# Kernel tuning notes

Hardware: AMD Instinct MI355X
Metric: run time of the kernel (lower is better)

The kernel has to match this reference:

```python
import jax, jax.numpy as jnp
import numpy as np

B, W, C, C2, K_DIV = 4, 64, 256, 256, 8
DPROJ = C // K_DIV  # 32


def setup_inputs() -> dict:
    key = jax.random.key(0)
    k1, k2, k3, k4 = jax.random.split(key, 4)
    x = jax.random.normal(k1, (B, W, W, C), dtype=jnp.float32)
    input_h = jax.random.normal(k2, (B, W, W, C2), dtype=jnp.float32)
    f_w = jax.random.normal(k3, (1, 1, C2, DPROJ), dtype=jnp.float32) * 0.05
    g_w = jax.random.normal(k4, (1, 1, C, DPROJ), dtype=jnp.float32) * 0.05
    return {"x": x, "input_h": input_h, "f_w": f_w, "g_w": g_w}


def reference(x, input_h, f_w, g_w):
    b, w, _, c = x.shape
    c2 = input_h.shape[-1]
    # 1x1 convs == channel matmuls
    f = jnp.einsum('bhwc,cd->bhwd', input_h, f_w[0, 0])   # [B,W,W,Dp]
    g = jnp.einsum('bhwc,cd->bhwd', x, g_w[0, 0])          # [B,W,W,Dp]
    gf = g.reshape(b, w * w, -1)                            # [B,N,Dp]
    ff = f.reshape(b, w * w, -1)                            # [B,N,Dp]
    s = jnp.einsum('bnd,bmd->bnm', gf, ff)                  # unscaled QK^T
    beta = jax.nn.softmax(s, axis=-1)
    hf = input_h.reshape(b, w * w, c2)                      # [B,N,C2]
    o = jnp.einsum('bnm,bmc->bnc', beta, hf).reshape(b, w, w, c2)
    return jnp.concatenate([o, x], axis=-1)                 # [B,W,W,C2+C]
```

## Files before the change

### kernel.cpp

```cpp
#include <hip/hip_runtime.h>
#include <hip/hip_bf16.h>

#define NB   4
#define NROW 4096
#define CIN  256
#define OUTC 512
#define DP   32
#define LOG2E 1.4426950408889634f

typedef __bf16 bf16x8 __attribute__((ext_vector_type(8)));
typedef float  f32x4  __attribute__((ext_vector_type(4)));
typedef float  f32x16 __attribute__((ext_vector_type(16)));
typedef ushort ushort8 __attribute__((ext_vector_type(8)));

#define MFMA32(a, b, c) __builtin_amdgcn_mfma_f32_32x32x16_bf16((a), (b), (c), 0, 0, 0)

__device__ __forceinline__ ushort f2bf(float x) {
  union { float f; unsigned u; } v; v.f = x;
  unsigned r = v.u + 0x7fffu + ((v.u >> 16) & 1u);
  return (ushort)(r >> 16);
}

__device__ __forceinline__ uint pack2(float a, float b) {
  __hip_bfloat162 h = __float22bfloat162_rn(float2{a, b});
  uint u; __builtin_memcpy(&u, &h, 4);
  return u;
}

__device__ __forceinline__ bf16x8 mk8(uint a, uint b, uint c, uint d) {
  uint tmp[4] = {a, b, c, d};
  bf16x8 r; __builtin_memcpy(&r, tmp, 16);
  return r;
}

__device__ __forceinline__ float fexp2(float x) {
  return __builtin_amdgcn_exp2f(x);
}

__device__ __forceinline__ void gload_lds16(const void* g, void* l) {
  __builtin_amdgcn_global_load_lds(
      (const __attribute__((address_space(1))) unsigned int*)g,
      (__attribute__((address_space(3))) unsigned int*)l, 16, 0, 0);
}


__global__ __launch_bounds__(256) void proj_mfma(
    const float* __restrict__ x, const float* __restrict__ h,
    const float* __restrict__ fw, const float* __restrict__ gw,
    ushort* __restrict__ Qb, ushort* __restrict__ Kb, ushort* __restrict__ Vw,
    float* __restrict__ out) {
  __shared__ ushort Ab[64 * 256];
  __shared__ ushort Wt[32 * 256];
  const int t = threadIdx.x;
  const int which = blockIdx.y;
  const float* in   = which ? h : x;
  const float* wsrc = which ? fw : gw;
  ushort* dst = which ? Kb : Qb;
  const float qsc = which ? 1.f : LOG2E;
  const int row0 = blockIdx.x * 64;

  {
    const float4* inp = (const float4*)(in + (size_t)row0 * CIN);
#pragma unroll
    for (int i = 0; i < 16; ++i) {
      const int idx = i * 256 + t;
      const int r = idx >> 6;
      const int c = (idx & 63) * 4;
      const float4 v = inp[idx];
      if (!which)
        ((float4*)(out + (size_t)(row0 + r) * OUTC + 256))[idx & 63] = v;
      ushort tmp[4] = {f2bf(v.x), f2bf(v.y), f2bf(v.z), f2bf(v.w)};
      const int slot = (c >> 3) ^ (r & 7);
      *(uint2*)&Ab[r * 256 + (slot << 3) + (c & 7)] = *(const uint2*)tmp;
    }
  }
  {
    const int d = t & 31;
    const int k0 = (t >> 5) * 32;
#pragma unroll 8
    for (int j = 0; j < 32; ++j)
      Wt[d * 256 + k0 + j] = f2bf(wsrc[(size_t)(k0 + j) * DP + d]);
  }
  __syncthreads();

  const int w = t >> 6, l = t & 63, lo = l & 15, hi = l >> 4;
  f32x4 acc[2];
  acc[0] = (f32x4){0.f, 0.f, 0.f, 0.f};
  acc[1] = (f32x4){0.f, 0.f, 0.f, 0.f};
  const int R = w * 16 + lo;
#pragma unroll
  for (int kk = 0; kk < 8; ++kk) {
    const int slot = (kk * 4 + hi) ^ (R & 7);
    const bf16x8 a = *(const bf16x8*)&Ab[R * 256 + (slot << 3)];
#pragma unroll
    for (int nt = 0; nt < 2; ++nt) {
      const bf16x8 bfr = *(const bf16x8*)&Wt[(nt * 16 + lo) * 256 + kk * 32 + hi * 8];
      acc[nt] = __builtin_amdgcn_mfma_f32_16x16x32_bf16(a, bfr, acc[nt], 0, 0, 0);
    }
  }
#pragma unroll
  for (int nt = 0; nt < 2; ++nt)
#pragma unroll
    for (int r = 0; r < 4; ++r)
      dst[(size_t)(row0 + w * 16 + hi * 4 + r) * DP + nt * 16 + lo] =
          f2bf(acc[nt][r] * qsc);

  if (which) {
    const int b = row0 >> 12;
    const int tile = (row0 & 4095) >> 6;
    const int c = t;
    ushort* vdst = Vw + (size_t)(b * 64 + tile) * 16384;
#pragma unroll
    for (int kt = 0; kt < 4; ++kt)
#pragma unroll
      for (int s2 = 0; s2 < 2; ++s2) {
        const int kbase = 16 * kt + 8 * (s2 ^ (c & 1));
        ushort tmp[8];
#pragma unroll
        for (int j = 0; j < 8; ++j) {
          const int slot = (c >> 3) ^ j;
          tmp[j] = Ab[(kbase + j) * 256 + (slot << 3) + (c & 7)];
        }
        *(ushort8*)(vdst + kt * 4096 + c * 16 + s2 * 8) = *(const ushort8*)tmp;
      }
  }
}

__global__ __launch_bounds__(256, 2) void attn32f(
    const ushort* __restrict__ Qb, const ushort* __restrict__ Kb,
    const ushort* __restrict__ Vw, float* __restrict__ pml,
    ushort* __restrict__ pacc) {
  __shared__ ushort Vt[2][16384];

  const int t  = threadIdx.x;
  const int w  = t >> 6;
  const int l  = t & 63;
  const int qq = l & 31;
  const int h  = l >> 5;

  const int bid = blockIdx.x;
  const int s   = bid & 3;
  const int b   = (bid >> 2) & 3;
  const int q0  = (bid >> 4) * 128 + w * 32;
  const size_t rbase = (size_t)b * NROW;

  bf16x8 qf0 = *(const bf16x8*)(Qb + (rbase + q0 + qq) * DP + h * 8);
  bf16x8 qf1 = *(const bf16x8*)(Qb + (rbase + q0 + qq) * DP + 16 + h * 8);

  f32x16 acc[8];
#pragma unroll
  for (int i = 0; i < 8; ++i) acc[i] = (f32x16){};
  float lsum = 0.f;

  const int tI0 = s * 16;
  const int vlane = qq * 32 + ((h ^ (qq & 1)) << 4);

  const int ko00 = qq * DP + h * 8;
  const int ko01 = qq * DP + 16 + h * 8;
  const int ko10 = (32 + qq) * DP + h * 8;
  const int ko11 = (32 + qq) * DP + 16 + h * 8;
  const ushort* kfp  = Kb + (rbase + (size_t)(tI0 + 1) * 64) * DP;
  const ushort* vsrc = Vw + (size_t)(b * 64 + tI0 + 1) * 16384;

  {
    const ushort* src0 = Vw + (size_t)(b * 64 + tI0) * 16384;
#pragma unroll
    for (int i = 0; i < 8; ++i)
      gload_lds16(src0 + (w * 8 + i) * 512 + l * 8, &Vt[0][(w * 8 + i) * 512]);
  }
  bf16x8 kf00, kf01, kf10, kf11;
  {
    const ushort* k0 = Kb + (rbase + (size_t)tI0 * 64) * DP;
    kf00 = *(const bf16x8*)(k0 + ko00);
    kf01 = *(const bf16x8*)(k0 + ko01);
    kf10 = *(const bf16x8*)(k0 + ko10);
    kf11 = *(const bf16x8*)(k0 + ko11);
  }
  __syncthreads();
  int cur = 0;

  for (int tt = 0; tt < 16; ++tt) {
    if (tt < 15) {
      ushort* dstl = &Vt[cur ^ 1][0];
#pragma unroll
      for (int i = 0; i < 8; ++i)
        gload_lds16(vsrc + (w * 8 + i) * 512 + l * 8, dstl + (w * 8 + i) * 512);
    }

    f32x16 st0 = (f32x16){}, st1 = (f32x16){};
    st0 = MFMA32(kf00, qf0, st0);
    st0 = MFMA32(kf01, qf1, st0);
    st1 = MFMA32(kf10, qf0, st1);
    st1 = MFMA32(kf11, qf1, st1);

#pragma unroll
    for (int i = 0; i < 16; ++i) st0[i] = fexp2(st0[i]);
    float s0;
    {
      float sm[8];
#pragma unroll
      for (int i = 0; i < 8; ++i) sm[i] = st0[i] + st0[i + 8];
#pragma unroll
      for (int d = 4; d >= 1; d >>= 1)
#pragma unroll
        for (int i = 0; i < d; ++i) sm[i] += sm[i + d];
      s0 = sm[0];
    }
    bf16x8 pb0, pb1;
    {
      const uint a00 = pack2(st0[0],  st0[1]),  a01 = pack2(st0[2],  st0[3]);
      const uint a10 = pack2(st0[4],  st0[5]),  a11 = pack2(st0[6],  st0[7]);
      const uint a20 = pack2(st0[8],  st0[9]),  a21 = pack2(st0[10], st0[11]);
      const uint a30 = pack2(st0[12], st0[13]), a31 = pack2(st0[14], st0[15]);
      auto p0 = __builtin_amdgcn_permlane32_swap(a00, a10, false, false);
      auto p1 = __builtin_amdgcn_permlane32_swap(a01, a11, false, false);
      auto p2 = __builtin_amdgcn_permlane32_swap(a20, a30, false, false);
      auto p3 = __builtin_amdgcn_permlane32_swap(a21, a31, false, false);
      pb0 = mk8(p0[0], p1[0], p0[1], p1[1]);
      pb1 = mk8(p2[0], p3[0], p2[1], p3[1]);
    }

    const char* vb = (const char*)&Vt[cur][0] + vlane;
    __builtin_amdgcn_s_setprio(1);
#pragma unroll
    for (int ct = 0; ct < 8; ++ct) {
      const bf16x8 v0 = *(const bf16x8*)(vb + ct * 1024);
      const bf16x8 v1 = *(const bf16x8*)(vb + 8192 + ct * 1024);
      acc[ct] = MFMA32(v0, pb0, acc[ct]);
      st1[2 * ct] = fexp2(st1[2 * ct]);
      acc[ct] = MFMA32(v1, pb1, acc[ct]);
      st1[2 * ct + 1] = fexp2(st1[2 * ct + 1]);
    }
    bf16x8 pb2, pb3;
    {
      const uint b00 = pack2(st1[0],  st1[1]),  b01 = pack2(st1[2],  st1[3]);
      const uint b10 = pack2(st1[4],  st1[5]),  b11 = pack2(st1[6],  st1[7]);
      const uint b20 = pack2(st1[8],  st1[9]),  b21 = pack2(st1[10], st1[11]);
      const uint b30 = pack2(st1[12], st1[13]), b31 = pack2(st1[14], st1[15]);
      auto p4 = __builtin_amdgcn_permlane32_swap(b00, b10, false, false);
      auto p5 = __builtin_amdgcn_permlane32_swap(b01, b11, false, false);
      auto p6 = __builtin_amdgcn_permlane32_swap(b20, b30, false, false);
      auto p7 = __builtin_amdgcn_permlane32_swap(b21, b31, false, false);
      pb2 = mk8(p4[0], p5[0], p4[1], p5[1]);
      pb3 = mk8(p6[0], p7[0], p6[1], p7[1]);
    }

    float s1 = 0.f;
#pragma unroll
    for (int ct = 0; ct < 8; ++ct) {
      const bf16x8 v2 = *(const bf16x8*)(vb + 16384 + ct * 1024);
      const bf16x8 v3 = *(const bf16x8*)(vb + 24576 + ct * 1024);
      acc[ct] = MFMA32(v2, pb2, acc[ct]);
      if (ct == 0) kf00 = *(const bf16x8*)(kfp + ko00);
      if (ct == 1) kf01 = *(const bf16x8*)(kfp + ko01);
      if (ct == 2) kf10 = *(const bf16x8*)(kfp + ko10);
      if (ct == 3) kf11 = *(const bf16x8*)(kfp + ko11);
      acc[ct] = MFMA32(v3, pb3, acc[ct]);
      s1 += st1[2 * ct] + st1[2 * ct + 1];
    }
    __builtin_amdgcn_s_setprio(0);
    lsum += s0 + s1;

    __syncthreads();
    cur ^= 1;
    kfp += 64 * DP;
    vsrc += 16384;
  }

  lsum += __shfl_xor(lsum, 32, 64);
  const size_t prow = rbase + q0 + qq;
  if (h == 0) pml[prow * 4 + s] = lsum;
  ushort* pr = pacc + (prow * 4 + s) * 256;
#pragma unroll
  for (int ct = 0; ct < 8; ++ct)
#pragma unroll
    for (int j = 0; j < 4; ++j) {
      uint2 d;
      d.x = pack2(acc[ct][4 * j], acc[ct][4 * j + 1]);
      d.y = pack2(acc[ct][4 * j + 2], acc[ct][4 * j + 3]);
      *(uint2*)&pr[ct * 32 + j * 8 + h * 4] = d;
    }
}

__global__ __launch_bounds__(256) void reduce_o(
    const float* __restrict__ pml, const ushort* __restrict__ pacc,
    float* __restrict__ out) {
  const int t = threadIdx.x;
  const int row = blockIdx.x * 8 + (t >> 5);
  const int c0 = (t & 31) * 8;

  const float L = pml[row * 4] + pml[row * 4 + 1] + pml[row * 4 + 2] + pml[row * 4 + 3];
  float o[8] = {0.f, 0.f, 0.f, 0.f, 0.f, 0.f, 0.f, 0.f};
#pragma unroll
  for (int s = 0; s < 4; ++s) {
    const bf16x8 a = *(const bf16x8*)(pacc + ((size_t)row * 4 + s) * 256 + c0);
#pragma unroll
    for (int i = 0; i < 8; ++i) o[i] += (float)a[i];
  }
  const float inv = 1.f / L;
  float4 o0 = {o[0] * inv, o[1] * inv, o[2] * inv, o[3] * inv};
  float4 o1 = {o[4] * inv, o[5] * inv, o[6] * inv, o[7] * inv};
  float4* op = (float4*)(out + (size_t)row * OUTC + c0);
  op[0] = o0; op[1] = o1;
}

__global__ __launch_bounds__(256) void proj_fb(
    const float* __restrict__ x, const float* __restrict__ h,
    const float* __restrict__ fw, const float* __restrict__ gw,
    float* __restrict__ out) {
  __shared__ float wl[8192];
  __shared__ float rows[8][260];
  const int t = threadIdx.x;
  const int which = blockIdx.y;
  const float* in = which ? h : x;
  const float* w  = which ? fw : gw;
  for (int i = t; i < 8192; i += 256) wl[i] = w[i];
  const int row0 = blockIdx.x * 32;
  const int d = t & 31, rl = t >> 5;
  for (int rp = 0; rp < 4; ++rp) {
    __syncthreads();
    for (int i = t; i < 2048; i += 256)
      rows[i >> 8][i & 255] = in[(long)(row0 + rp * 8 + (i >> 8)) * CIN + (i & 255)];
    __syncthreads();
    float a = 0.f;
#pragma unroll 8
    for (int c = 0; c < 256; ++c) a = fmaf(rows[rl][c], wl[c * 32 + d], a);
    const long row = row0 + rp * 8 + rl;
    ((ushort*)(out + row * OUTC + 256))[which * 32 + d] = f2bf(a);
  }
}

__global__ __launch_bounds__(256) void attn_fb(
    const float* __restrict__ h, float* __restrict__ out) {
  __shared__ alignas(16) ushort Vt[256][72];
  __shared__ alignas(16) ushort Pl[4][16][72];
  const int t = threadIdx.x;
  const int w = t >> 6, l = t & 63, lo = l & 15, hi = l >> 4;
  const int bid = blockIdx.x;
  const int b = (bid >> 1) & 3;
  const int qb = ((bid >> 3) << 1) | (bid & 1);
  const int q0 = qb * 64;
  const long rowbase = (long)b * NROW;
  const ushort* gslot = (const ushort*)(out + (rowbase + q0 + w * 16 + lo) * OUTC + 256);
  const bf16x8 qf = *(const bf16x8*)(gslot + hi * 8);
  f32x4 acc[16];
#pragma unroll
  for (int i = 0; i < 16; ++i) acc[i] = (f32x4){0.f, 0.f, 0.f, 0.f};
  float mrow[4] = {-1e30f, -1e30f, -1e30f, -1e30f};
  float lsum[4] = {0.f, 0.f, 0.f, 0.f};
  for (int k0 = 0; k0 < NROW; k0 += 64) {
    bf16x8 kf[4];
#pragma unroll
    for (int kt = 0; kt < 4; ++kt) {
      const ushort* fslot =
          (const ushort*)(out + (rowbase + k0 + kt * 16 + lo) * OUTC + 256) + 32;
      kf[kt] = *(const bf16x8*)(fslot + hi * 8);
    }
    __syncthreads();
    {
      const float* hp = h + (rowbase + k0) * CIN + t;
#pragma unroll
      for (int g8 = 0; g8 < 8; ++g8) {
        ushort tmp[8];
#pragma unroll
        for (int i = 0; i < 8; ++i) tmp[i] = f2bf(hp[(g8 * 8 + i) * CIN]);
        *(bf16x8*)&Vt[t][g8 * 8] = *(const bf16x8*)tmp;
      }
    }
    __syncthreads();
    f32x4 sv[4];
#pragma unroll
    for (int kt = 0; kt < 4; ++kt)
      sv[kt] = __builtin_amdgcn_mfma_f32_16x16x32_bf16(
          qf, kf[kt], (f32x4){0.f, 0.f, 0.f, 0.f}, 0, 0, 0);
    float alpha[4];
    bool upd = false;
#pragma unroll
    for (int r = 0; r < 4; ++r) {
      float m4 = fmaxf(fmaxf(sv[0][r], sv[1][r]), fmaxf(sv[2][r], sv[3][r]));
#pragma unroll
      for (int off = 1; off < 16; off <<= 1) m4 = fmaxf(m4, __shfl_xor(m4, off, 64));
      const float mn = fmaxf(mrow[r], m4);
      alpha[r] = __expf(mrow[r] - mn);
      upd |= (mn > mrow[r]);
      mrow[r] = mn;
    }
    if (__any(upd)) {
#pragma unroll
      for (int ct = 0; ct < 16; ++ct)
#pragma unroll
        for (int r = 0; r < 4; ++r) acc[ct][r] *= alpha[r];
#pragma unroll
      for (int r = 0; r < 4; ++r) lsum[r] *= alpha[r];
    }
#pragma unroll
    for (int r = 0; r < 4; ++r) {
      float ps = 0.f;
#pragma unroll
      for (int kt = 0; kt < 4; ++kt) {
        const float p = __expf(sv[kt][r] - mrow[r]);
        sv[kt][r] = p;
        ps += p;
      }
#pragma unroll
      for (int off = 1; off < 16; off <<= 1) ps += __shfl_xor(ps, off, 64);
      lsum[r] += ps;
    }
#pragma unroll
    for (int kt = 0; kt < 4; ++kt)
#pragma unroll
      for (int r = 0; r < 4; ++r)
        Pl[w][hi * 4 + r][kt * 16 + lo] = f2bf(sv[kt][r]);
    asm volatile("s_waitcnt lgkmcnt(0)" ::: "memory");
    const bf16x8 pa0 = *(const bf16x8*)&Pl[w][lo][hi * 8];
    const bf16x8 pa1 = *(const bf16x8*)&Pl[w][lo][32 + hi * 8];
#pragma unroll
    for (int ct = 0; ct < 16; ++ct) {
      const bf16x8 v0 = *(const bf16x8*)&Vt[ct * 16 + lo][hi * 8];
      const bf16x8 v1 = *(const bf16x8*)&Vt[ct * 16 + lo][32 + hi * 8];
      acc[ct] = __builtin_amdgcn_mfma_f32_16x16x32_bf16(pa0, v0, acc[ct], 0, 0, 0);
      acc[ct] = __builtin_amdgcn_mfma_f32_16x16x32_bf16(pa1, v1, acc[ct], 0, 0, 0);
    }
  }
#pragma unroll
  for (int r = 0; r < 4; ++r) {
    const float inv = 1.f / lsum[r];
    float* orow = out + (rowbase + q0 + w * 16 + hi * 4 + r) * OUTC;
#pragma unroll
    for (int ct = 0; ct < 16; ++ct) orow[ct * 16 + lo] = acc[ct][r] * inv;
  }
}

__global__ __launch_bounds__(256) void concat_fb(
    const float4* __restrict__ x, float4* __restrict__ out) {
  const int idx = blockIdx.x * 256 + threadIdx.x;
  const int row = idx >> 6, c4 = idx & 63;
  out[row * 128 + 64 + c4] = x[idx];
}

extern "C" void kernel_launch(void* const* d_in, const int* in_sizes, int n_in,
                              void* d_out, int out_size, void* d_ws, size_t ws_size,
                              hipStream_t stream) {
  const float* x  = (const float*)d_in[0];
  const float* h  = (const float*)d_in[1];
  const float* fw = (const float*)d_in[2];
  const float* gw = (const float*)d_in[3];
  float* out = (float*)d_out;

  const size_t rows = (size_t)NB * NROW;
  const size_t base = 10ull * 1024 * 1024;
  const size_t need = base + rows * 4 * 8 + rows * 4 * 512;

  if (ws_size >= need) {
    ushort* Qw = (ushort*)d_ws;
    ushort* Kw = Qw + (1ull << 19);
    ushort* Vw = Kw + (1ull << 19);
    float*  pml  = (float*)((char*)d_ws + base);
    ushort* pacc = (ushort*)((char*)d_ws + base + rows * 4 * 8);

    proj_mfma<<<dim3(256, 2), 256, 0, stream>>>(x, h, fw, gw, Qw, Kw, Vw, out);
    attn32f<<<512, 256, 0, stream>>>(Qw, Kw, Vw, pml, pacc);
    reduce_o<<<2048, 256, 0, stream>>>(pml, pacc, out);
  } else {
    proj_fb<<<dim3(512, 2), 256, 0, stream>>>(x, h, fw, gw, out);
    attn_fb<<<256, 256, 0, stream>>>(h, out);
    concat_fb<<<4096, 256, 0, stream>>>((const float4*)x, (float4*)out);
  }
}
```

Before: 73.78 us.

## Fuse split-K reduction into attention kernel via last-block atomic counter

Removes the separate reduce_o launch. Each attention block bumps a per-(batch, query-block) atomic counter after writing its partial sums, and the last of the four split blocks reduces the partials and writes the normalized output. The counters are zeroed in the projection kernel. This saves one kernel launch and the gap between launches, at the cost of threadfences and an atomic per block, and a serialized reduction tail done by a quarter of the blocks.

```diff
diff --git a/kernel.cpp b/kernel.cpp
--- a/kernel.cpp
+++ b/kernel.cpp
@@ -29,7 +29,7 @@
 
 __device__ __forceinline__ bf16x8 mk8(uint a, uint b, uint c, uint d) {
   uint tmp[4] = {a, b, c, d};
-  bf16x8 r; __builtin_memcpy(&r, tmp, 16);
+  bf16x8 r; __builtin_memcpy(&r, tmp, 4 * 4);
   return r;
 }
 
@@ -43,12 +43,30 @@
       (__attribute__((address_space(3))) unsigned int*)l, 16, 0, 0);
 }
 
+__device__ __forceinline__ void reduce_rows(
+    int row, int c0, const float* __restrict__ pml,
+    const ushort* __restrict__ pacc, float* __restrict__ out) {
+  const float L = pml[row * 4] + pml[row * 4 + 1] + pml[row * 4 + 2] + pml[row * 4 + 3];
+  float o[8] = {0.f, 0.f, 0.f, 0.f, 0.f, 0.f, 0.f, 0.f};
+#pragma unroll
+  for (int s = 0; s < 4; ++s) {
+    const bf16x8 a = *(const bf16x8*)(pacc + ((size_t)row * 4 + s) * 256 + c0);
+#pragma unroll
+    for (int i = 0; i < 8; ++i) o[i] += (float)a[i];
+  }
+  const float inv = 1.f / L;
+  float4 o0 = {o[0] * inv, o[1] * inv, o[2] * inv, o[3] * inv};
+  float4 o1 = {o[4] * inv, o[5] * inv, o[6] * inv, o[7] * inv};
+  float4* op = (float4*)(out + (size_t)row * OUTC + c0);
+  op[0] = o0; op[1] = o1;
+}
+
 
 __global__ __launch_bounds__(256) void proj_mfma(
     const float* __restrict__ x, const float* __restrict__ h,
     const float* __restrict__ fw, const float* __restrict__ gw,
     ushort* __restrict__ Qb, ushort* __restrict__ Kb, ushort* __restrict__ Vw,
-    float* __restrict__ out) {
+    int* __restrict__ cnt, float* __restrict__ out) {
   __shared__ ushort Ab[64 * 256];
   __shared__ ushort Wt[32 * 256];
   const int t = threadIdx.x;
@@ -58,6 +76,8 @@
   ushort* dst = which ? Kb : Qb;
   const float qsc = which ? 1.f : LOG2E;
   const int row0 = blockIdx.x * 64;
+
+  if (which && blockIdx.x == 0 && t < 128) cnt[t] = 0;
 
   {
     const float4* inp = (const float4*)(in + (size_t)row0 * CIN);
@@ -129,8 +149,10 @@
 __global__ __launch_bounds__(256, 2) void attn32f(
     const ushort* __restrict__ Qb, const ushort* __restrict__ Kb,
     const ushort* __restrict__ Vw, float* __restrict__ pml,
-    ushort* __restrict__ pacc) {
+    ushort* __restrict__ pacc, int* __restrict__ cnt,
+    float* __restrict__ out) {
   __shared__ ushort Vt[2][16384];
+  __shared__ int lastFlag;
 
   const int t  = threadIdx.x;
   const int w  = t >> 6;
@@ -141,7 +163,8 @@
   const int bid = blockIdx.x;
   const int s   = bid & 3;
   const int b   = (bid >> 2) & 3;
-  const int q0  = (bid >> 4) * 128 + w * 32;
+  const int qblk = bid >> 4;
+  const int q0  = qblk * 128 + w * 32;
   const size_t rbase = (size_t)b * NROW;
 
   bf16x8 qf0 = *(const bf16x8*)(Qb + (rbase + q0 + qq) * DP + h * 8);
@@ -280,28 +303,20 @@
       d.y = pack2(acc[ct][4 * j + 2], acc[ct][4 * j + 3]);
       *(uint2*)&pr[ct * 32 + j * 8 + h * 4] = d;
     }
-}
-
-__global__ __launch_bounds__(256) void reduce_o(
-    const float* __restrict__ pml, const ushort* __restrict__ pacc,
-    float* __restrict__ out) {
-  const int t = threadIdx.x;
-  const int row = blockIdx.x * 8 + (t >> 5);
-  const int c0 = (t & 31) * 8;
-
-  const float L = pml[row * 4] + pml[row * 4 + 1] + pml[row * 4 + 2] + pml[row * 4 + 3];
-  float o[8] = {0.f, 0.f, 0.f, 0.f, 0.f, 0.f, 0.f, 0.f};
-#pragma unroll
-  for (int s = 0; s < 4; ++s) {
-    const bf16x8 a = *(const bf16x8*)(pacc + ((size_t)row * 4 + s) * 256 + c0);
-#pragma unroll
-    for (int i = 0; i < 8; ++i) o[i] += (float)a[i];
-  }
-  const float inv = 1.f / L;
-  float4 o0 = {o[0] * inv, o[1] * inv, o[2] * inv, o[3] * inv};
-  float4 o1 = {o[4] * inv, o[5] * inv, o[6] * inv, o[7] * inv};
-  float4* op = (float4*)(out + (size_t)row * OUTC + c0);
-  op[0] = o0; op[1] = o1;
+
+  __threadfence();
+  if (t == 0)
+    lastFlag = (atomicAdd(&cnt[b * 32 + qblk], 1) == 3);
+  __syncthreads();
+  if (lastFlag) {
+    __threadfence();
+    const int rowg = b * NROW + qblk * 128;
+    const int c0 = (l & 31) * 8;
+    const int rl = t >> 5;
+#pragma unroll
+    for (int rep = 0; rep < 16; ++rep)
+      reduce_rows(rowg + rep * 8 + rl, c0, pml, pacc, out);
+  }
 }
 
 __global__ __launch_bounds__(256) void proj_fb(
@@ -449,7 +464,7 @@
 
   const size_t rows = (size_t)NB * NROW;
   const size_t base = 10ull * 1024 * 1024;
-  const size_t need = base + rows * 4 * 8 + rows * 4 * 512;
+  const size_t need = base + rows * 4 * 8 + rows * 4 * 512 + 512;
 
   if (ws_size >= need) {
     ushort* Qw = (ushort*)d_ws;
@@ -457,10 +472,10 @@
     ushort* Vw = Kw + (1ull << 19);
     float*  pml  = (float*)((char*)d_ws + base);
     ushort* pacc = (ushort*)((char*)d_ws + base + rows * 4 * 8);
-
-    proj_mfma<<<dim3(256, 2), 256, 0, stream>>>(x, h, fw, gw, Qw, Kw, Vw, out);
-    attn32f<<<512, 256, 0, stream>>>(Qw, Kw, Vw, pml, pacc);
-    reduce_o<<<2048, 256, 0, stream>>>(pml, pacc, out);
+    int*    cnt  = (int*)((char*)d_ws + base + rows * 4 * 8 + rows * 4 * 512);
+
+    proj_mfma<<<dim3(256, 2), 256, 0, stream>>>(x, h, fw, gw, Qw, Kw, Vw, cnt, out);
+    attn32f<<<512, 256, 0, stream>>>(Qw, Kw, Vw, pml, pacc, cnt, out);
   } else {
     proj_fb<<<dim3(512, 2), 256, 0, stream>>>(x, h, fw, gw, out);
     attn_fb<<<256, 256, 0, stream>>>(h, out);
```

After: 205.0 us. 2.78x slower.

## Split attention block across channel halves and single-buffer V tile

Applied to the files above, without the earlier changes.

The attention kernel now gives each block 64 query rows instead of 128, with the four waves split into two query groups times two channel halves. Each wave accumulates 128 output channels instead of 256, which halves the accumulator registers, and the grid doubles to 1024 blocks. The V tile in shared memory drops from double to single buffering so occupancy can rise to 3 blocks per CU. The cost is that V loads no longer overlap with compute, an extra barrier is added per iteration, and the QK^T and exp work is done twice, once per channel-half wave.

```diff
diff --git a/kernel.cpp b/kernel.cpp
--- a/kernel.cpp
+++ b/kernel.cpp
@@ -126,34 +126,36 @@
   }
 }
 
-__global__ __launch_bounds__(256, 2) void attn32f(
+__global__ __launch_bounds__(256, 3) void attn64c(
     const ushort* __restrict__ Qb, const ushort* __restrict__ Kb,
     const ushort* __restrict__ Vw, float* __restrict__ pml,
     ushort* __restrict__ pacc) {
-  __shared__ ushort Vt[2][16384];
+  __shared__ ushort Vt[16384];
 
   const int t  = threadIdx.x;
   const int w  = t >> 6;
   const int l  = t & 63;
   const int qq = l & 31;
   const int h  = l >> 5;
+  const int qs  = w & 1;
+  const int chh = w >> 1;
 
   const int bid = blockIdx.x;
   const int s   = bid & 3;
   const int b   = (bid >> 2) & 3;
-  const int q0  = (bid >> 4) * 128 + w * 32;
+  const int q0  = (bid >> 4) * 64 + qs * 32;
   const size_t rbase = (size_t)b * NROW;
 
   bf16x8 qf0 = *(const bf16x8*)(Qb + (rbase + q0 + qq) * DP + h * 8);
   bf16x8 qf1 = *(const bf16x8*)(Qb + (rbase + q0 + qq) * DP + 16 + h * 8);
 
-  f32x16 acc[8];
-#pragma unroll
-  for (int i = 0; i < 8; ++i) acc[i] = (f32x16){};
+  f32x16 acc[4];
+#pragma unroll
+  for (int i = 0; i < 4; ++i) acc[i] = (f32x16){};
   float lsum = 0.f;
 
   const int tI0 = s * 16;
-  const int vlane = qq * 32 + ((h ^ (qq & 1)) << 4);
+  const int vlane = chh * 4096 + qq * 32 + ((h ^ (qq & 1)) << 4);
 
   const int ko00 = qq * DP + h * 8;
   const int ko01 = qq * DP + 16 + h * 8;
@@ -166,7 +168,7 @@
     const ushort* src0 = Vw + (size_t)(b * 64 + tI0) * 16384;
 #pragma unroll
     for (int i = 0; i < 8; ++i)
-      gload_lds16(src0 + (w * 8 + i) * 512 + l * 8, &Vt[0][(w * 8 + i) * 512]);
+      gload_lds16(src0 + (w * 8 + i) * 512 + l * 8, &Vt[(w * 8 + i) * 512]);
   }
   bf16x8 kf00, kf01, kf10, kf11;
   {
@@ -177,16 +179,8 @@
     kf11 = *(const bf16x8*)(k0 + ko11);
   }
   __syncthreads();
-  int cur = 0;
 
   for (int tt = 0; tt < 16; ++tt) {
-    if (tt < 15) {
-      ushort* dstl = &Vt[cur ^ 1][0];
-#pragma unroll
-      for (int i = 0; i < 8; ++i)
-        gload_lds16(vsrc + (w * 8 + i) * 512 + l * 8, dstl + (w * 8 + i) * 512);
-    }
-
     f32x16 st0 = (f32x16){}, st1 = (f32x16){};
     st0 = MFMA32(kf00, qf0, st0);
     st0 = MFMA32(kf01, qf1, st0);
@@ -220,16 +214,20 @@
       pb1 = mk8(p2[0], p3[0], p2[1], p3[1]);
     }
 
-    const char* vb = (const char*)&Vt[cur][0] + vlane;
+    __syncthreads();
+
+    const char* vb = (const char*)&Vt[0] + vlane;
     __builtin_amdgcn_s_setprio(1);
 #pragma unroll
-    for (int ct = 0; ct < 8; ++ct) {
+    for (int ct = 0; ct < 4; ++ct) {
       const bf16x8 v0 = *(const bf16x8*)(vb + ct * 1024);
       const bf16x8 v1 = *(const bf16x8*)(vb + 8192 + ct * 1024);
       acc[ct] = MFMA32(v0, pb0, acc[ct]);
-      st1[2 * ct] = fexp2(st1[2 * ct]);
+      st1[4 * ct]     = fexp2(st1[4 * ct]);
+      st1[4 * ct + 1] = fexp2(st1[4 * ct + 1]);
       acc[ct] = MFMA32(v1, pb1, acc[ct]);
-      st1[2 * ct + 1] = fexp2(st1[2 * ct + 1]);
+      st1[4 * ct + 2] = fexp2(st1[4 * ct + 2]);
+      st1[4 * ct + 3] = fexp2(st1[4 * ct + 3]);
     }
     bf16x8 pb2, pb3;
     {
@@ -247,7 +245,7 @@
 
     float s1 = 0.f;
 #pragma unroll
-    for (int ct = 0; ct < 8; ++ct) {
+    for (int ct = 0; ct < 4; ++ct) {
       const bf16x8 v2 = *(const bf16x8*)(vb + 16384 + ct * 1024);
       const bf16x8 v3 = *(const bf16x8*)(vb + 24576 + ct * 1024);
       acc[ct] = MFMA32(v2, pb2, acc[ct]);
@@ -256,23 +254,28 @@
       if (ct == 2) kf10 = *(const bf16x8*)(kfp + ko10);
       if (ct == 3) kf11 = *(const bf16x8*)(kfp + ko11);
       acc[ct] = MFMA32(v3, pb3, acc[ct]);
-      s1 += st1[2 * ct] + st1[2 * ct + 1];
+      s1 += (st1[4 * ct] + st1[4 * ct + 1]) + (st1[4 * ct + 2] + st1[4 * ct + 3]);
     }
     __builtin_amdgcn_s_setprio(0);
     lsum += s0 + s1;
 
     __syncthreads();
-    cur ^= 1;
+
+    if (tt < 15) {
+#pragma unroll
+      for (int i = 0; i < 8; ++i)
+        gload_lds16(vsrc + (w * 8 + i) * 512 + l * 8, &Vt[(w * 8 + i) * 512]);
+    }
     kfp += 64 * DP;
     vsrc += 16384;
   }
 
   lsum += __shfl_xor(lsum, 32, 64);
   const size_t prow = rbase + q0 + qq;
-  if (h == 0) pml[prow * 4 + s] = lsum;
-  ushort* pr = pacc + (prow * 4 + s) * 256;
-#pragma unroll
-  for (int ct = 0; ct < 8; ++ct)
+  if (h == 0 && chh == 0) pml[prow * 4 + s] = lsum;
+  ushort* pr = pacc + (prow * 4 + s) * 256 + chh * 128;
+#pragma unroll
+  for (int ct = 0; ct < 4; ++ct)
 #pragma unroll
     for (int j = 0; j < 4; ++j) {
       uint2 d;
@@ -459,7 +462,7 @@
     ushort* pacc = (ushort*)((char*)d_ws + base + rows * 4 * 8);
 
     proj_mfma<<<dim3(256, 2), 256, 0, stream>>>(x, h, fw, gw, Qw, Kw, Vw, out);
-    attn32f<<<512, 256, 0, stream>>>(Qw, Kw, Vw, pml, pacc);
+    attn64c<<<1024, 256, 0, stream>>>(Qw, Kw, Vw, pml, pacc);
     reduce_o<<<2048, 256, 0, stream>>>(pml, pacc, out);
   } else {
     proj_fb<<<dim3(512, 2), 256, 0, stream>>>(x, h, fw, gw, out);
```

Result: slower. 86.15 us (+16.8%).
